# Kernel tuning notes

Measured on AMD Instinct MI355X. Metric: run time of the kernel, lower is better.

The kernel has to match this reference:

```python
import jax, jax.numpy as jnp
import numpy as np

N = 50000      # nodes
F_IN = 128     # in_features
F_OUT = 128    # out_features
E = 800000     # edges (avg degree 16)


def setup_inputs() -> dict:
    key = jax.random.key(0)
    k = jax.random.split(key, 6)
    x = jax.random.normal(k[0], (N, F_IN), dtype=jnp.float32)
    h0 = jax.random.normal(k[1], (N, F_IN), dtype=jnp.float32)
    edge_row = jax.random.randint(k[2], (E,), 0, N, dtype=jnp.int32)
    edge_col = jax.random.randint(k[3], (E,), 0, N, dtype=jnp.int32)
    # normalized-Laplacian-like positive weights
    edge_val = jax.random.uniform(k[4], (E,), dtype=jnp.float32)
    stdv = 1.0 / np.sqrt(F_OUT)
    weight = jax.random.uniform(k[5], (F_IN, F_OUT), dtype=jnp.float32,
                                minval=-stdv, maxval=stdv)
    return {
        "input": x,
        "h0": h0,
        "edge_row": edge_row,
        "edge_col": edge_col,
        "edge_val": edge_val,
        "weight": weight,
        "lamda": jnp.float32(0.5),
        "alpha": jnp.float32(0.1),
        "l": 4,  # layer index (python int)
    }


def reference(input, h0, edge_row, edge_col, edge_val, weight, lamda, alpha, l):
    # theta = log(lamda / l + 1)
    theta = jnp.log(lamda / l + 1.0)
    # hi = spmm(G, input): gather source features, scale by edge value, scatter-add to rows
    msgs = edge_val[:, None] * input[edge_col]              # [E, F]
    hi = jax.ops.segment_sum(msgs, edge_row, num_segments=N)  # [N, F]
    # variant=False: support == r == (1-alpha)*hi + alpha*h0
    support = (1.0 - alpha) * hi + alpha * h0
    out = theta * (support @ weight) + (1.0 - theta) * support
    # residual=True
    out = out + input
    return out
```

## Files before the change

kernel.cpp:

```cpp
#include <hip/hip_runtime.h>
#include <math.h>

#define NF 128
#define SCAN_B 1024


__global__ __launch_bounds__(256) void hist_kernel(
    const int* __restrict__ erow, int* __restrict__ cnt, int E_) {
    int e = blockIdx.x * 256 + threadIdx.x;
    if (e < E_) atomicAdd(&cnt[erow[e]], 1);
}

__global__ __launch_bounds__(SCAN_B) void scanA_kernel(
    const int* __restrict__ cnt, int* __restrict__ bsum, int N_) {
    __shared__ int buf[SCAN_B];
    int t = threadIdx.x;
    int i = blockIdx.x * SCAN_B + t;
    buf[t] = (i < N_) ? cnt[i] : 0;
    __syncthreads();
    for (int d = SCAN_B / 2; d > 0; d >>= 1) {
        if (t < d) buf[t] += buf[t + d];
        __syncthreads();
    }
    if (t == 0) bsum[blockIdx.x] = buf[0];
}

__global__ __launch_bounds__(SCAN_B) void scanC_kernel(
    const int* __restrict__ cnt, const int* __restrict__ bsum,
    int* __restrict__ off, int* __restrict__ pos, int N_, int nb) {
    __shared__ int buf[SCAN_B];
    __shared__ int bpre_sh;
    int t = threadIdx.x;
    if (t < 64) {
        int v0 = (t < nb) ? bsum[t] : 0;
        int v = v0;
        for (int d = 1; d < 64; d <<= 1) {
            int u = __shfl_up(v, d, 64);
            if (t >= d) v += u;
        }
        if (t == (int)blockIdx.x) bpre_sh = v - v0;
        if (blockIdx.x == 0 && t == nb - 1) off[N_] = v;
    }
    int i = blockIdx.x * SCAN_B + t;
    int v = (i < N_) ? cnt[i] : 0;
    buf[t] = v;
    __syncthreads();
    for (int d = 1; d < SCAN_B; d <<= 1) {
        int add = (t >= d) ? buf[t - d] : 0;
        __syncthreads();
        buf[t] += add;
        __syncthreads();
    }
    if (i < N_) {
        int o = bpre_sh + buf[t] - v;
        off[i] = o;
        pos[i] = o;
    }
}

__global__ __launch_bounds__(256) void fill_kernel(
    const int* __restrict__ erow, const int* __restrict__ ecol,
    const float* __restrict__ evalv, int* __restrict__ pos,
    int2* __restrict__ epack, int E_) {
    int e = blockIdx.x * 256 + threadIdx.x;
    if (e >= E_) return;
    int p = atomicAdd(&pos[erow[e]], 1);
    int2 pk;
    pk.x = ecol[e];
    pk.y = __float_as_int(evalv[e]);
    epack[p] = pk;
}


__global__ __launch_bounds__(256) void spmm_kernel(
    const float* __restrict__ x, const float* __restrict__ h0,
    const int* __restrict__ off, const int2* __restrict__ epack,
    float* __restrict__ sup, const float* __restrict__ alpha_p, int N_) {
    int w = (blockIdx.x * 256 + threadIdx.x) >> 6;
    if (w >= N_) return;
    int lane = threadIdx.x & 63;
    int sub  = lane & 31;
    int half = lane >> 5;
    int s = off[w], e = off[w + 1];
    float4 acc = {0.f, 0.f, 0.f, 0.f};
    int i = s + half;
    for (; i + 2 < e; i += 4) {
        int2 e0 = epack[i];
        int2 e1 = epack[i + 2];
        float v0 = __int_as_float(e0.y);
        float v1 = __int_as_float(e1.y);
        float4 a = *((const float4*)(x + (size_t)e0.x * NF) + sub);
        float4 b = *((const float4*)(x + (size_t)e1.x * NF) + sub);
        acc.x += v0 * a.x + v1 * b.x;
        acc.y += v0 * a.y + v1 * b.y;
        acc.z += v0 * a.z + v1 * b.z;
        acc.w += v0 * a.w + v1 * b.w;
    }
    for (; i < e; i += 2) {
        int2 e0 = epack[i];
        float v0 = __int_as_float(e0.y);
        float4 a = *((const float4*)(x + (size_t)e0.x * NF) + sub);
        acc.x += v0 * a.x;
        acc.y += v0 * a.y;
        acc.z += v0 * a.z;
        acc.w += v0 * a.w;
    }
    acc.x += __shfl_xor(acc.x, 32, 64);
    acc.y += __shfl_xor(acc.y, 32, 64);
    acc.z += __shfl_xor(acc.z, 32, 64);
    acc.w += __shfl_xor(acc.w, 32, 64);
    if (half == 0) {
        float alpha = *alpha_p;
        float oma = 1.0f - alpha;
        float4 h = *((const float4*)(h0 + (size_t)w * NF) + sub);
        float4 o;
        o.x = oma * acc.x + alpha * h.x;
        o.y = oma * acc.y + alpha * h.y;
        o.z = oma * acc.z + alpha * h.z;
        o.w = oma * acc.w + alpha * h.w;
        *((float4*)(sup + (size_t)w * NF) + sub) = o;
    }
}


__global__ __launch_bounds__(256) void gemm_epilogue_kernel(
    const float* __restrict__ sup, const float* __restrict__ W,
    const float* __restrict__ inp, float* __restrict__ out,
    const float* __restrict__ lamda_p, const int* __restrict__ l_p, int n_rows) {
    __shared__ float Ws[NF * NF];
    int tid = threadIdx.x;
    for (int i = tid; i < NF * NF / 4; i += 256)
        ((float4*)Ws)[i] = ((const float4*)W)[i];
    __syncthreads();

    float theta = logf((*lamda_p) / (float)(*l_p) + 1.0f);
    float omt = 1.0f - theta;

    int m0   = blockIdx.x * 32;
    int tcol = tid & 31;
    int trow = tid >> 5;
    int n    = tcol * 4;
    int mbase = m0 + trow * 4;

    int mr[4];
#pragma unroll
    for (int r = 0; r < 4; r++) {
        int m = mbase + r;
        mr[r] = (m < n_rows) ? m : (n_rows - 1);
    }

    float acc[4][4] = {};
    for (int k = 0; k < NF; k += 4) {
        float4 srow[4];
#pragma unroll
        for (int r = 0; r < 4; r++)
            srow[r] = *(const float4*)&sup[(size_t)mr[r] * NF + k];
#pragma unroll
        for (int kk = 0; kk < 4; kk++) {
            float4 w = *(const float4*)&Ws[(k + kk) * NF + n];
#pragma unroll
            for (int r = 0; r < 4; r++) {
                float s = (&srow[r].x)[kk];
                acc[r][0] += s * w.x;
                acc[r][1] += s * w.y;
                acc[r][2] += s * w.z;
                acc[r][3] += s * w.w;
            }
        }
    }

#pragma unroll
    for (int r = 0; r < 4; r++) {
        int m = mbase + r;
        if (m >= n_rows) break;
        float4 sv = *(const float4*)&sup[(size_t)m * NF + n];
        float4 iv = *(const float4*)&inp[(size_t)m * NF + n];
        float4 o;
        o.x = theta * acc[r][0] + omt * sv.x + iv.x;
        o.y = theta * acc[r][1] + omt * sv.y + iv.y;
        o.z = theta * acc[r][2] + omt * sv.z + iv.z;
        o.w = theta * acc[r][3] + omt * sv.w + iv.w;
        *(float4*)&out[(size_t)m * NF + n] = o;
    }
}

extern "C" void kernel_launch(void* const* d_in, const int* in_sizes, int n_in,
                              void* d_out, int out_size, void* d_ws, size_t ws_size,
                              hipStream_t stream) {
    const float* x       = (const float*)d_in[0];
    const float* h0      = (const float*)d_in[1];
    const int*   erow    = (const int*)d_in[2];
    const int*   ecol    = (const int*)d_in[3];
    const float* evalv   = (const float*)d_in[4];
    const float* W       = (const float*)d_in[5];
    const float* lamda_p = (const float*)d_in[6];
    const float* alpha_p = (const float*)d_in[7];
    const int*   l_p     = (const int*)d_in[8];

    int N_ = in_sizes[0] / NF;
    int E_ = in_sizes[2];
    int nb = (N_ + SCAN_B - 1) / SCAN_B;

    char* ws = (char*)d_ws;
    size_t o = 0;
    auto alloc = [&](size_t bytes) { char* p = ws + o; o = (o + bytes + 255) & ~(size_t)255; return p; };
    float* sup   = (float*)alloc((size_t)N_ * NF * sizeof(float));
    int*   cnt   = (int*)  alloc((size_t)N_ * sizeof(int));
    int*   off   = (int*)  alloc((size_t)(N_ + 1) * sizeof(int));
    int*   pos   = (int*)  alloc((size_t)N_ * sizeof(int));
    int2*  epack = (int2*) alloc((size_t)E_ * sizeof(int2));
    int*   bsum  = (int*)  alloc((size_t)nb * sizeof(int));

    float* out = (float*)d_out;

    hipMemsetAsync(cnt, 0, (size_t)N_ * sizeof(int), stream);
    hist_kernel<<<(E_ + 255) / 256, 256, 0, stream>>>(erow, cnt, E_);
    scanA_kernel<<<nb, SCAN_B, 0, stream>>>(cnt, bsum, N_);
    scanC_kernel<<<nb, SCAN_B, 0, stream>>>(cnt, bsum, off, pos, N_, nb);
    fill_kernel<<<(E_ + 255) / 256, 256, 0, stream>>>(erow, ecol, evalv, pos, epack, E_);

    int blocks = (N_ * 64 + 255) / 256;
    spmm_kernel<<<blocks, 256, 0, stream>>>(x, h0, off, epack, sup, alpha_p, N_);

    gemm_epilogue_kernel<<<(N_ + 31) / 32, 256, 0, stream>>>(
        sup, W, x, out, lamda_p, l_p, N_);
}
```

Baseline: 294.6 us.

## Gather SpMM source features from a bf16 copy of the input

Adds a conversion kernel that writes a bf16 copy of the input features, and makes the SpMM gather from that copy. Each wave now splits into four groups of 16 lanes, and each lane unpacks 8 bf16 values per load. This halves the bytes moved by the random row gathers, which dominate the SpMM. In exchange it adds an extra pass that reads and writes the full feature matrix, and it introduces bf16 rounding error into the aggregated features.

Measured after the change: 275.9 us. 1.07x faster.

```diff
diff --git a/kernel.cpp b/kernel.cpp
--- a/kernel.cpp
+++ b/kernel.cpp
@@ -3,6 +3,27 @@
 
 #define NF 128
 #define SCAN_B 1024
+
+
+__device__ __forceinline__ unsigned short f2bf(float f) {
+    unsigned int u = __float_as_uint(f);
+    u = (u + 0x7fffu + ((u >> 16) & 1u)) >> 16;
+    return (unsigned short)u;
+}
+
+__global__ __launch_bounds__(256) void cvt_kernel(
+    const float* __restrict__ x, uint* __restrict__ xb, int n8) {
+    int i = blockIdx.x * 256 + threadIdx.x;
+    if (i >= n8) return;
+    float4 a = ((const float4*)x)[i * 2];
+    float4 b = ((const float4*)x)[i * 2 + 1];
+    uint4 o;
+    o.x = (uint)f2bf(a.x) | ((uint)f2bf(a.y) << 16);
+    o.y = (uint)f2bf(a.z) | ((uint)f2bf(a.w) << 16);
+    o.z = (uint)f2bf(b.x) | ((uint)f2bf(b.y) << 16);
+    o.w = (uint)f2bf(b.z) | ((uint)f2bf(b.w) << 16);
+    ((uint4*)xb)[i] = o;
+}
 
 
 __global__ __launch_bounds__(256) void hist_kernel(
@@ -72,53 +93,70 @@
 }
 
 
+#define UNPK_FMA(u, v, a0, a1)                         \
+    a0 += (v) * __uint_as_float((u) << 16);            \
+    a1 += (v) * __uint_as_float((u) & 0xffff0000u);
+
 __global__ __launch_bounds__(256) void spmm_kernel(
-    const float* __restrict__ x, const float* __restrict__ h0,
+    const unsigned short* __restrict__ xb, const float* __restrict__ h0,
     const int* __restrict__ off, const int2* __restrict__ epack,
     float* __restrict__ sup, const float* __restrict__ alpha_p, int N_) {
     int w = (blockIdx.x * 256 + threadIdx.x) >> 6;
     if (w >= N_) return;
     int lane = threadIdx.x & 63;
-    int sub  = lane & 31;
-    int half = lane >> 5;
+    int g    = lane >> 4;
+    int seg  = lane & 15;
     int s = off[w], e = off[w + 1];
-    float4 acc = {0.f, 0.f, 0.f, 0.f};
-    int i = s + half;
-    for (; i + 2 < e; i += 4) {
+    float acc[8] = {};
+    int i = s + g;
+    for (; i + 4 < e; i += 8) {
         int2 e0 = epack[i];
-        int2 e1 = epack[i + 2];
+        int2 e1 = epack[i + 4];
         float v0 = __int_as_float(e0.y);
         float v1 = __int_as_float(e1.y);
-        float4 a = *((const float4*)(x + (size_t)e0.x * NF) + sub);
-        float4 b = *((const float4*)(x + (size_t)e1.x * NF) + sub);
-        acc.x += v0 * a.x + v1 * b.x;
-        acc.y += v0 * a.y + v1 * b.y;
-        acc.z += v0 * a.z + v1 * b.z;
-        acc.w += v0 * a.w + v1 * b.w;
-    }
-    for (; i < e; i += 2) {
+        uint4 a = *(const uint4*)(xb + (size_t)e0.x * NF + seg * 8);
+        uint4 b = *(const uint4*)(xb + (size_t)e1.x * NF + seg * 8);
+        UNPK_FMA(a.x, v0, acc[0], acc[1]);
+        UNPK_FMA(a.y, v0, acc[2], acc[3]);
+        UNPK_FMA(a.z, v0, acc[4], acc[5]);
+        UNPK_FMA(a.w, v0, acc[6], acc[7]);
+        UNPK_FMA(b.x, v1, acc[0], acc[1]);
+        UNPK_FMA(b.y, v1, acc[2], acc[3]);
+        UNPK_FMA(b.z, v1, acc[4], acc[5]);
+        UNPK_FMA(b.w, v1, acc[6], acc[7]);
+    }
+    if (i < e) {
         int2 e0 = epack[i];
         float v0 = __int_as_float(e0.y);
-        float4 a = *((const float4*)(x + (size_t)e0.x * NF) + sub);
-        acc.x += v0 * a.x;
-        acc.y += v0 * a.y;
-        acc.z += v0 * a.z;
-        acc.w += v0 * a.w;
-    }
-    acc.x += __shfl_xor(acc.x, 32, 64);
-    acc.y += __shfl_xor(acc.y, 32, 64);
-    acc.z += __shfl_xor(acc.z, 32, 64);
-    acc.w += __shfl_xor(acc.w, 32, 64);
-    if (half == 0) {
+        uint4 a = *(const uint4*)(xb + (size_t)e0.x * NF + seg * 8);
+        UNPK_FMA(a.x, v0, acc[0], acc[1]);
+        UNPK_FMA(a.y, v0, acc[2], acc[3]);
+        UNPK_FMA(a.z, v0, acc[4], acc[5]);
+        UNPK_FMA(a.w, v0, acc[6], acc[7]);
+    }
+#pragma unroll
+    for (int j = 0; j < 8; j++) {
+        acc[j] += __shfl_xor(acc[j], 16, 64);
+        acc[j] += __shfl_xor(acc[j], 32, 64);
+    }
+    if (g == 0) {
         float alpha = *alpha_p;
         float oma = 1.0f - alpha;
-        float4 h = *((const float4*)(h0 + (size_t)w * NF) + sub);
-        float4 o;
-        o.x = oma * acc.x + alpha * h.x;
-        o.y = oma * acc.y + alpha * h.y;
-        o.z = oma * acc.z + alpha * h.z;
-        o.w = oma * acc.w + alpha * h.w;
-        *((float4*)(sup + (size_t)w * NF) + sub) = o;
+        const float* h = h0 + (size_t)w * NF + seg * 8;
+        float4 ha = *(const float4*)h;
+        float4 hb = *(const float4*)(h + 4);
+        float4 o1, o2;
+        o1.x = oma * acc[0] + alpha * ha.x;
+        o1.y = oma * acc[1] + alpha * ha.y;
+        o1.z = oma * acc[2] + alpha * ha.z;
+        o1.w = oma * acc[3] + alpha * ha.w;
+        o2.x = oma * acc[4] + alpha * hb.x;
+        o2.y = oma * acc[5] + alpha * hb.y;
+        o2.z = oma * acc[6] + alpha * hb.z;
+        o2.w = oma * acc[7] + alpha * hb.w;
+        float* d = sup + (size_t)w * NF + seg * 8;
+        *(float4*)d = o1;
+        *(float4*)(d + 4) = o2;
     }
 }
 
@@ -205,6 +243,7 @@
     size_t o = 0;
     auto alloc = [&](size_t bytes) { char* p = ws + o; o = (o + bytes + 255) & ~(size_t)255; return p; };
     float* sup   = (float*)alloc((size_t)N_ * NF * sizeof(float));
+    unsigned short* xb = (unsigned short*)alloc((size_t)N_ * NF * 2);
     int*   cnt   = (int*)  alloc((size_t)N_ * sizeof(int));
     int*   off   = (int*)  alloc((size_t)(N_ + 1) * sizeof(int));
     int*   pos   = (int*)  alloc((size_t)N_ * sizeof(int));
@@ -213,6 +252,9 @@
 
     float* out = (float*)d_out;
 
+    int n8 = N_ * NF / 8;
+    cvt_kernel<<<(n8 + 255) / 256, 256, 0, stream>>>(x, (uint*)xb, n8);
+
     hipMemsetAsync(cnt, 0, (size_t)N_ * sizeof(int), stream);
     hist_kernel<<<(E_ + 255) / 256, 256, 0, stream>>>(erow, cnt, E_);
     scanA_kernel<<<nb, SCAN_B, 0, stream>>>(cnt, bsum, N_);
@@ -220,7 +262,7 @@
     fill_kernel<<<(E_ + 255) / 256, 256, 0, stream>>>(erow, ecol, evalv, pos, epack, E_);
 
     int blocks = (N_ * 64 + 255) / 256;
-    spmm_kernel<<<blocks, 256, 0, stream>>>(x, h0, off, epack, sup, alpha_p, N_);
+    spmm_kernel<<<blocks, 256, 0, stream>>>(xb, h0, off, epack, sup, alpha_p, N_);
 
     gemm_epilogue_kernel<<<(N_ + 31) / 32, 256, 0, stream>>>(
         sup, W, x, out, lamda_p, l_p, N_);
```
